# Kernel tuning notes

Measured on AMD Instinct MI355X. Metric: run time of the kernel, lower is better.

## Reference

```python
import jax, jax.numpy as jnp
import numpy as np

B, CIN, COUT, N = 8, 64, 64, 4096
MODES, L, M = 64, 100, 20


def _cc_nodes_weights(m):
    # Clenshaw-Curtis nodes cos(k*pi/n) and weights on [-1, 1]
    n = m - 1
    k = np.arange(m)
    nodes = np.cos(np.pi * k / n)
    v = np.ones(m)
    for j in range(1, n // 2 + 1):
        b = 1.0 if 2 * j == n else 2.0
        v -= b / (4.0 * j * j - 1.0) * np.cos(2.0 * j * k * np.pi / n)
    w = 2.0 * v / n
    w[0] *= 0.5
    w[-1] *= 0.5
    return nodes, w


def setup_inputs() -> dict:
    key = jax.random.key(0)
    k1, k2, k3 = jax.random.split(key, 3)
    scale = 1.0 / (CIN * COUT)
    x = jax.random.normal(k1, (B, CIN, N), dtype=jnp.float32)
    w_real = scale * jax.random.uniform(k2, (CIN, COUT, MODES), dtype=jnp.float32)
    w_imag = scale * jax.random.uniform(k3, (CIN, COUT, MODES), dtype=jnp.float32)
    return {"x": x, "w_real": w_real, "w_imag": w_imag}


def _forward(x, w_real, w_imag):
    b, c, n = x.shape
    t = jnp.linspace(0.0, 1.0, n)
    f = np.fft.fftfreq(n, d=1.0 / n).astype(np.float32)  # integer freqs, fft order
    nodes, cw = _cc_nodes_weights(M)

    # ---- CFT: X(f) = sum_{segments l, cheb nodes k} w_lk * x(t_lk) * exp(-2i*pi*f*t_lk)
    h = 0.5 / L                               # segment half-width on [0,1]
    cents = (np.arange(L) + 0.5) / L
    t_nodes = (cents[:, None] + h * nodes[None, :]).ravel().astype(np.float32)  # (L*M,)
    wts = np.broadcast_to(h * cw, (L, M)).ravel().astype(np.float32)            # (L*M,)
    tq = jnp.asarray(t_nodes)
    # interpolate each (b, c) signal onto the Chebyshev quadrature nodes
    xs = jax.vmap(lambda s: jnp.interp(tq, t, s))(x.reshape(b * c, n))  # (BC, LM)
    phase = -2.0 * jnp.pi * jnp.asarray(f)[:, None] * tq[None, :]       # (N, LM)
    E = jnp.exp(1j * phase).astype(jnp.complex64) * jnp.asarray(wts)[None, :]
    x_cft = (xs.astype(jnp.complex64) @ E.T).reshape(b, c, n)           # (B, Cin, N)

    # ---- spectral channel mixing on lowest MODES fft-order frequencies
    w = (w_real + 1j * w_imag).astype(jnp.complex64)
    out_low = jnp.einsum('bix,iox->box', x_cft[:, :, :MODES], w)
    out_ft = jnp.concatenate(
        [out_low, jnp.zeros((b, COUT, n - MODES), dtype=jnp.complex64)], axis=-1)

    # ---- ICFT: x(t) = int X(f) exp(+2i*pi*f*t) df via the same segment quadrature
    order = np.argsort(f)
    f_sorted = f[order]
    cs = out_ft[:, :, jnp.asarray(order)].reshape(b * COUT, n)
    fa, fb = float(f_sorted[0]), float(f_sorted[-1])
    hf = (fb - fa) / (2.0 * L)
    fc = fa + (np.arange(L) + 0.5) * (fb - fa) / L
    f_nodes = (fc[:, None] + hf * nodes[None, :]).ravel().astype(np.float32)
    wfs = np.broadcast_to(hf * cw, (L, M)).ravel().astype(np.float32)
    fq = jnp.asarray(f_nodes)
    fs = jnp.asarray(f_sorted)
    ci = jax.vmap(lambda cv: jnp.interp(fq, fs, cv.real)
                  + 1j * jnp.interp(fq, fs, cv.imag))(cs)               # (BC, LM)
    phase2 = 2.0 * jnp.pi * fq[:, None] * t[None, :]                     # (LM, N)
    E2 = jnp.exp(1j * phase2).astype(jnp.complex64) * jnp.asarray(wfs)[:, None]
    return (ci.astype(jnp.complex64) @ E2).real.reshape(b, COUT, n)


def reference(x, w_real, w_imag):
    return _forward(x, w_real, w_imag)
```

## Files before the change

### kernel.cpp

```cpp
#include <hip/hip_runtime.h>


#define NN 4096
#define C1_19 0.9863613034027223
#define NS3 33
#define NSP 40

#define OFF_XRE 0
#define OFF_XIM 32768
#define OFF_Z   65536

__device__ __forceinline__ float sin_rev(float r) { return __builtin_amdgcn_sinf(r); }
__device__ __forceinline__ float cos_rev(float r) { return __builtin_amdgcn_cosf(r); }

__device__ __forceinline__ void build_tables(double* nd, double* cwd, int t) {
    if (t == 0) {
        nd[0] = 1.0; nd[1] = C1_19;
        for (int k = 2; k < 20; ++k) nd[k] = 2.0 * C1_19 * nd[k - 1] - nd[k - 2];
    }
    __syncthreads();
    if (t < 20) {
        double v = 1.0;
        for (int j = 1; j <= 9; ++j) {
            int q = (2 * j * t) % 38; if (q > 19) q = 38 - q;
            v -= 2.0 / (4.0 * j * j - 1.0) * nd[q];
        }
        double w = 2.0 * v / 19.0;
        if (t == 0 || t == 19) w *= 0.5;
        cwd[t] = w;
    }
}

__global__ __launch_bounds__(256) void k_cft(const float* __restrict__ x,
                                             float* __restrict__ ws) {
    __shared__ double nd[20], cwd[20];
    __shared__ __align__(16) float xs[NN];
    __shared__ __align__(16) float xq[2000];
    __shared__ __align__(16) float Fri[20][64][2];
    __shared__ float red[4][64][2];
    const int t = threadIdx.x;
    const int bc = blockIdx.x;
    build_tables(nd, cwd, t);
#pragma unroll
    for (int it = 0; it < 4; ++it) {
        int c4 = it * 256 + t;
        *(float4*)&xs[c4 * 4] = *(const float4*)&x[(size_t)bc * NN + c4 * 4];
    }
    __syncthreads();
    for (int idx = t; idx < 1280; idx += 256) {
        int k = idx >> 6, m = idx & 63;
        double r = -0.005 * nd[k] * (double)m;
        r -= floor(r);
        float fr = (float)r;
        float w = (float)(0.005 * cwd[k]);
        Fri[k][m][0] = w * cos_rev(fr);
        Fri[k][m][1] = w * sin_rev(fr);
    }
#pragma unroll
    for (int it = 0; it < 8; ++it) {
        int node = it * 256 + t;
        if (node < 2000) {
            int l = node / 20, k = node - l * 20;
            double tq = 0.005 * ((double)(2 * l + 1) + nd[k]);
            double sf = tq * 4095.0;
            int i = (int)sf; if (i > 4094) i = 4094;
            double a = sf - (double)i;
            if (a < 0.0) a = 0.0; if (a > 1.0) a = 1.0;
            float af = (float)a;
            xq[node] = (1.f - af) * xs[i] + af * xs[i + 1];
        }
    }
    __syncthreads();
    const int m = t & 63, grp = t >> 6;
    float Fre[20], Fim[20];
#pragma unroll
    for (int k = 0; k < 20; ++k) {
        Fre[k] = Fri[k][m][0];
        Fim[k] = Fri[k][m][1];
    }
    float ar = 0.f, ai = 0.f;
    for (int l = grp * 25; l < grp * 25 + 25; ++l) {
        const float4* q4 = (const float4*)&xq[l * 20];
        float ur = 0.f, ui = 0.f;
#pragma unroll
        for (int c = 0; c < 5; ++c) {
            float4 q = q4[c];
            ur += q.x * Fre[c * 4]     + q.y * Fre[c * 4 + 1]
                + q.z * Fre[c * 4 + 2] + q.w * Fre[c * 4 + 3];
            ui += q.x * Fim[c * 4]     + q.y * Fim[c * 4 + 1]
                + q.z * Fim[c * 4 + 2] + q.w * Fim[c * 4 + 3];
        }
        double r = -(double)(m * (2 * l + 1)) / 200.0;
        r -= floor(r);
        float fr = (float)r;
        float tr = cos_rev(fr), ti = sin_rev(fr);
        ar += tr * ur - ti * ui;
        ai += tr * ui + ti * ur;
    }
    red[grp][m][0] = ar;
    red[grp][m][1] = ai;
    __syncthreads();
    if (t < 64) {
        float sr = (red[0][t][0] + red[1][t][0]) + (red[2][t][0] + red[3][t][0]);
        float si = (red[0][t][1] + red[1][t][1]) + (red[2][t][1] + red[3][t][1]);
        ws[OFF_XRE + (size_t)bc * 64 + t] = sr;
        ws[OFF_XIM + (size_t)bc * 64 + t] = si;
    }
}

__global__ __launch_bounds__(256) void k_mixZ(const float* __restrict__ wr,
                                              const float* __restrict__ wi,
                                              float* __restrict__ ws) {
    __shared__ double nd[20], cwd[20];
    __shared__ float part[4][2][64];
    __shared__ float yt[2][64];
    __shared__ float sw0[NS3], sw1[NS3];
    __shared__ int   si0[NS3], si1[NS3];
    const int t = threadIdx.x;
    const int b = blockIdx.x >> 6, o = blockIdx.x & 63;
    build_tables(nd, cwd, t);
    __syncthreads();
    if (t < NS3) {
        int l = (t < 2) ? 49 : (t < 22 ? 50 : 51);
        int k = (t < 2) ? t : (t < 22 ? t - 2 : t - 13);
        double fq = -2048.0 + ((double)l + 0.5) * 40.95 + 20.475 * nd[k];
        int m0 = (int)floor(fq);
        float fr = (float)(fq - (double)m0);
        sw0[t] = (m0 >= 0 && m0 <= 63) ? (1.f - fr) : 0.f;
        sw1[t] = (m0 + 1 >= 0 && m0 + 1 <= 63) ? fr : 0.f;
        si0[t] = min(max(m0, 0), 63);
        si1[t] = min(max(m0 + 1, 0), 63);
    }
    const int m = t & 63, grp = t >> 6;
    float yr = 0.f, yi = 0.f;
#pragma unroll 4
    for (int i = grp * 16; i < grp * 16 + 16; ++i) {
        float xr = ws[OFF_XRE + (size_t)(b * 64 + i) * 64 + m];
        float xi = ws[OFF_XIM + (size_t)(b * 64 + i) * 64 + m];
        float a = wr[((size_t)i * 64 + o) * 64 + m];
        float c = wi[((size_t)i * 64 + o) * 64 + m];
        yr += xr * a - xi * c;
        yi += xr * c + xi * a;
    }
    part[grp][0][m] = yr;
    part[grp][1][m] = yi;
    __syncthreads();
    if (t < 128) {
        int pr = t >> 6, mm = t & 63;
        yt[pr][mm] = ((part[0][pr][mm] + part[1][pr][mm]) +
                      (part[2][pr][mm] + part[3][pr][mm]));
    }
    __syncthreads();
    if (t < 2 * NS3) {
        int p = t >= NS3, s = t - p * NS3;
        float z = sw0[s] * yt[p][si0[s]] + sw1[s] * yt[p][si1[s]];
        ws[OFF_Z + (size_t)p * 512 * NSP + ((size_t)b * 64 + o) * NSP + s] = z;
    } else if (t < 2 * NS3 + 14) {
        int u = t - 2 * NS3;
        int p = u / 7, s = NS3 + u % 7;
        ws[OFF_Z + (size_t)p * 512 * NSP + ((size_t)b * 64 + o) * NSP + s] = 0.f;
    }
}

__global__ __launch_bounds__(256) void k_stage3(const float* __restrict__ ws,
                                                float* __restrict__ out) {
    __shared__ double nd[20], cwd[20];
    __shared__ double sfq[NS3];
    __shared__ float  swf[NS3];
    __shared__ __align__(16) float zt[2][64][41];
    __shared__ __align__(16) float e2[2][NSP][64];
    const int t = threadIdx.x;
    const int jt = blockIdx.x, pc = blockIdx.y;
    build_tables(nd, cwd, t);
    __syncthreads();
    if (t < NS3) {
        int l = (t < 2) ? 49 : (t < 22 ? 50 : 51);
        int k = (t < 2) ? t : (t < 22 ? t - 2 : t - 13);
        sfq[t] = -2048.0 + ((double)l + 0.5) * 40.95 + 20.475 * nd[k];
        swf[t] = (float)(20.475 * cwd[k]);
    }
    for (int idx = t; idx < 2 * 64 * NSP; idx += 256) {
        int part = idx / (64 * NSP), rem = idx % (64 * NSP);
        int row = rem / NSP, s = rem % NSP;
        zt[part][row][s] =
            ws[OFF_Z + (size_t)part * 512 * NSP + ((size_t)pc * 64 + row) * NSP + s];
    }
    __syncthreads();
    const double inv4095 = 1.0 / 4095.0;
    for (int idx = t; idx < NSP * 64; idx += 256) {
        int s = idx >> 6, jl = idx & 63;
        float cr = 0.f, ci = 0.f;
        if (s < NS3) {
            double ph = sfq[s] * ((double)(jt * 64 + jl) * inv4095);
            ph -= floor(ph);
            float fr = (float)ph;
            cr = swf[s] * cos_rev(fr);
            ci = swf[s] * sin_rev(fr);
        }
        e2[0][s][jl] = cr;
        e2[1][s][jl] = ci;
    }
    __syncthreads();
    const int jg = t & 15, pg = t >> 4;
    float acc[4][4] = {{0.f}};
    for (int s0 = 0; s0 < NSP; s0 += 8) {
        float zr[4][8], zi[4][8];
#pragma unroll
        for (int p = 0; p < 4; ++p)
#pragma unroll
            for (int u = 0; u < 8; ++u) {
                zr[p][u] = zt[0][pg * 4 + p][s0 + u];
                zi[p][u] = zt[1][pg * 4 + p][s0 + u];
            }
#pragma unroll
        for (int u = 0; u < 8; ++u) {
            const float4 er = *(const float4*)&e2[0][s0 + u][jg * 4];
            const float4 ei = *(const float4*)&e2[1][s0 + u][jg * 4];
#pragma unroll
            for (int p = 0; p < 4; ++p) {
                acc[p][0] += zr[p][u] * er.x - zi[p][u] * ei.x;
                acc[p][1] += zr[p][u] * er.y - zi[p][u] * ei.y;
                acc[p][2] += zr[p][u] * er.z - zi[p][u] * ei.z;
                acc[p][3] += zr[p][u] * er.w - zi[p][u] * ei.w;
            }
        }
    }
#pragma unroll
    for (int p = 0; p < 4; ++p) {
        float4 r;
        r.x = acc[p][0]; r.y = acc[p][1]; r.z = acc[p][2]; r.w = acc[p][3];
        *(float4*)&out[(size_t)(pc * 64 + pg * 4 + p) * NN + jt * 64 + jg * 4] = r;
    }
}

extern "C" void kernel_launch(void* const* d_in, const int* in_sizes, int n_in,
                              void* d_out, int out_size, void* d_ws, size_t ws_size,
                              hipStream_t stream) {
    const float* x  = (const float*)d_in[0];
    const float* wr = (const float*)d_in[1];
    const float* wi = (const float*)d_in[2];
    float* out = (float*)d_out;
    float* ws  = (float*)d_ws;
    (void)in_sizes; (void)n_in; (void)out_size; (void)ws_size;

    k_cft<<<512, 256, 0, stream>>>(x, ws);
    k_mixZ<<<512, 256, 0, stream>>>(wr, wi, ws);
    k_stage3<<<dim3(64, 8), 256, 0, stream>>>(ws, out);
}
```

Measured before the change: 31.10 us.

## Fuse channel-mixing and inverse-transform kernels with per-batch atomic counter barrier

Merges the mixing kernel and the inverse transform kernel into a single launch. Each block first computes its Z slice, then increments a per-batch counter and spins until all 64 blocks of that batch have arrived before running the inverse transform. This removes one kernel launch and its inter-kernel gap. Shared memory for the two phases is overlaid with a union. The counters are reset from the first kernel. Separately, the CFT twiddle phase now uses an integer modulo instead of double-precision floor. The spin barrier depends on all 512 blocks being co-resident and on correct memory visibility, since the stores and loads use only relaxed ordering.

```diff
diff --git a/kernel.cpp b/kernel.cpp
--- a/kernel.cpp
+++ b/kernel.cpp
@@ -9,6 +9,7 @@
 #define OFF_XRE 0
 #define OFF_XIM 32768
 #define OFF_Z   65536
+#define OFF_CNT 106496
 
 __device__ __forceinline__ float sin_rev(float r) { return __builtin_amdgcn_sinf(r); }
 __device__ __forceinline__ float cos_rev(float r) { return __builtin_amdgcn_cosf(r); }
@@ -40,6 +41,9 @@
     __shared__ float red[4][64][2];
     const int t = threadIdx.x;
     const int bc = blockIdx.x;
+    if (bc == 0 && t < 8)
+        __hip_atomic_store((unsigned*)ws + OFF_CNT + t * 16, 0u,
+                           __ATOMIC_RELAXED, __HIP_MEMORY_SCOPE_SYSTEM);
     build_tables(nd, cwd, t);
 #pragma unroll
     for (int it = 0; it < 4; ++it) {
@@ -90,10 +94,9 @@
             ui += q.x * Fim[c * 4]     + q.y * Fim[c * 4 + 1]
                 + q.z * Fim[c * 4 + 2] + q.w * Fim[c * 4 + 3];
         }
-        double r = -(double)(m * (2 * l + 1)) / 200.0;
-        r -= floor(r);
-        float fr = (float)r;
-        float tr = cos_rev(fr), ti = sin_rev(fr);
+        int u = (m * (2 * l + 1)) % 200;
+        float fr = (float)u * 0.005f;
+        float tr = cos_rev(fr), ti = -sin_rev(fr);
         ar += tr * ur - ti * ui;
         ai += tr * ui + ti * ur;
     }
@@ -108,22 +111,30 @@
     }
 }
 
-__global__ __launch_bounds__(256) void k_mixZ(const float* __restrict__ wr,
-                                              const float* __restrict__ wi,
-                                              float* __restrict__ ws) {
+struct PhC { float part[4][2][64]; float yt[2][64]; };
+struct PhD { float zt[2][64][41]; float e2[2][NSP][64]; };
+union SU2 { PhC c; PhD d; };
+
+__global__ __launch_bounds__(256) void k_mixicft(const float* __restrict__ wr,
+                                                 const float* __restrict__ wi,
+                                                 float* __restrict__ ws,
+                                                 float* __restrict__ out) {
+    __shared__ SU2 su;
     __shared__ double nd[20], cwd[20];
-    __shared__ float part[4][2][64];
-    __shared__ float yt[2][64];
     __shared__ float sw0[NS3], sw1[NS3];
     __shared__ int   si0[NS3], si1[NS3];
+    __shared__ double sfq[NS3];
+    __shared__ float  swf[NS3];
     const int t = threadIdx.x;
-    const int b = blockIdx.x >> 6, o = blockIdx.x & 63;
+    const int b = blockIdx.x >> 6, u = blockIdx.x & 63;
     build_tables(nd, cwd, t);
     __syncthreads();
     if (t < NS3) {
         int l = (t < 2) ? 49 : (t < 22 ? 50 : 51);
         int k = (t < 2) ? t : (t < 22 ? t - 2 : t - 13);
         double fq = -2048.0 + ((double)l + 0.5) * 40.95 + 20.475 * nd[k];
+        sfq[t] = fq;
+        swf[t] = (float)(20.475 * cwd[k]);
         int m0 = (int)floor(fq);
         float fr = (float)(fq - (double)m0);
         sw0[t] = (m0 >= 0 && m0 <= 63) ? (1.f - fr) : 0.f;
@@ -131,105 +142,104 @@
         si0[t] = min(max(m0, 0), 63);
         si1[t] = min(max(m0 + 1, 0), 63);
     }
-    const int m = t & 63, grp = t >> 6;
-    float yr = 0.f, yi = 0.f;
+    {
+        const int o = u;
+        const int m = t & 63, grp = t >> 6;
+        float yr = 0.f, yi = 0.f;
 #pragma unroll 4
-    for (int i = grp * 16; i < grp * 16 + 16; ++i) {
-        float xr = ws[OFF_XRE + (size_t)(b * 64 + i) * 64 + m];
-        float xi = ws[OFF_XIM + (size_t)(b * 64 + i) * 64 + m];
-        float a = wr[((size_t)i * 64 + o) * 64 + m];
-        float c = wi[((size_t)i * 64 + o) * 64 + m];
-        yr += xr * a - xi * c;
-        yi += xr * c + xi * a;
-    }
-    part[grp][0][m] = yr;
-    part[grp][1][m] = yi;
-    __syncthreads();
-    if (t < 128) {
-        int pr = t >> 6, mm = t & 63;
-        yt[pr][mm] = ((part[0][pr][mm] + part[1][pr][mm]) +
-                      (part[2][pr][mm] + part[3][pr][mm]));
-    }
-    __syncthreads();
-    if (t < 2 * NS3) {
-        int p = t >= NS3, s = t - p * NS3;
-        float z = sw0[s] * yt[p][si0[s]] + sw1[s] * yt[p][si1[s]];
-        ws[OFF_Z + (size_t)p * 512 * NSP + ((size_t)b * 64 + o) * NSP + s] = z;
-    } else if (t < 2 * NS3 + 14) {
-        int u = t - 2 * NS3;
-        int p = u / 7, s = NS3 + u % 7;
-        ws[OFF_Z + (size_t)p * 512 * NSP + ((size_t)b * 64 + o) * NSP + s] = 0.f;
-    }
-}
-
-__global__ __launch_bounds__(256) void k_stage3(const float* __restrict__ ws,
-                                                float* __restrict__ out) {
-    __shared__ double nd[20], cwd[20];
-    __shared__ double sfq[NS3];
-    __shared__ float  swf[NS3];
-    __shared__ __align__(16) float zt[2][64][41];
-    __shared__ __align__(16) float e2[2][NSP][64];
-    const int t = threadIdx.x;
-    const int jt = blockIdx.x, pc = blockIdx.y;
-    build_tables(nd, cwd, t);
-    __syncthreads();
-    if (t < NS3) {
-        int l = (t < 2) ? 49 : (t < 22 ? 50 : 51);
-        int k = (t < 2) ? t : (t < 22 ? t - 2 : t - 13);
-        sfq[t] = -2048.0 + ((double)l + 0.5) * 40.95 + 20.475 * nd[k];
-        swf[t] = (float)(20.475 * cwd[k]);
-    }
-    for (int idx = t; idx < 2 * 64 * NSP; idx += 256) {
-        int part = idx / (64 * NSP), rem = idx % (64 * NSP);
-        int row = rem / NSP, s = rem % NSP;
-        zt[part][row][s] =
-            ws[OFF_Z + (size_t)part * 512 * NSP + ((size_t)pc * 64 + row) * NSP + s];
-    }
-    __syncthreads();
-    const double inv4095 = 1.0 / 4095.0;
-    for (int idx = t; idx < NSP * 64; idx += 256) {
-        int s = idx >> 6, jl = idx & 63;
-        float cr = 0.f, ci = 0.f;
-        if (s < NS3) {
-            double ph = sfq[s] * ((double)(jt * 64 + jl) * inv4095);
-            ph -= floor(ph);
-            float fr = (float)ph;
-            cr = swf[s] * cos_rev(fr);
-            ci = swf[s] * sin_rev(fr);
-        }
-        e2[0][s][jl] = cr;
-        e2[1][s][jl] = ci;
-    }
-    __syncthreads();
-    const int jg = t & 15, pg = t >> 4;
-    float acc[4][4] = {{0.f}};
-    for (int s0 = 0; s0 < NSP; s0 += 8) {
-        float zr[4][8], zi[4][8];
-#pragma unroll
-        for (int p = 0; p < 4; ++p)
-#pragma unroll
-            for (int u = 0; u < 8; ++u) {
-                zr[p][u] = zt[0][pg * 4 + p][s0 + u];
-                zi[p][u] = zt[1][pg * 4 + p][s0 + u];
+        for (int i = grp * 16; i < grp * 16 + 16; ++i) {
+            float xr = ws[OFF_XRE + (size_t)(b * 64 + i) * 64 + m];
+            float xi = ws[OFF_XIM + (size_t)(b * 64 + i) * 64 + m];
+            float a = wr[((size_t)i * 64 + o) * 64 + m];
+            float c = wi[((size_t)i * 64 + o) * 64 + m];
+            yr += xr * a - xi * c;
+            yi += xr * c + xi * a;
+        }
+        su.c.part[grp][0][m] = yr;
+        su.c.part[grp][1][m] = yi;
+        __syncthreads();
+        if (t < 128) {
+            int pr = t >> 6, mm = t & 63;
+            su.c.yt[pr][mm] = ((su.c.part[0][pr][mm] + su.c.part[1][pr][mm]) +
+                               (su.c.part[2][pr][mm] + su.c.part[3][pr][mm]));
+        }
+        __syncthreads();
+        if (t < 2 * NS3) {
+            int p = t >= NS3, s = t - p * NS3;
+            float z = sw0[s] * su.c.yt[p][si0[s]] + sw1[s] * su.c.yt[p][si1[s]];
+            __hip_atomic_store(&ws[OFF_Z + (size_t)p * 512 * NSP +
+                                   ((size_t)b * 64 + o) * NSP + s],
+                               z, __ATOMIC_RELAXED, __HIP_MEMORY_SCOPE_SYSTEM);
+        } else if (t < 2 * NS3 + 14) {
+            int q = t - 2 * NS3;
+            int p = q / 7, s = NS3 + q % 7;
+            __hip_atomic_store(&ws[OFF_Z + (size_t)p * 512 * NSP +
+                                   ((size_t)b * 64 + o) * NSP + s],
+                               0.f, __ATOMIC_RELAXED, __HIP_MEMORY_SCOPE_SYSTEM);
+        }
+    }
+    __syncthreads();
+    if (t == 0) {
+        unsigned* cnt = (unsigned*)ws + OFF_CNT + b * 16;
+        __hip_atomic_fetch_add(cnt, 1u, __ATOMIC_RELAXED, __HIP_MEMORY_SCOPE_AGENT);
+        while (__hip_atomic_load(cnt, __ATOMIC_RELAXED, __HIP_MEMORY_SCOPE_AGENT) < 64u)
+            __builtin_amdgcn_s_sleep(4);
+    }
+    __syncthreads();
+    {
+        const int jt = u, pc = b;
+        for (int idx = t; idx < 2 * 64 * NSP; idx += 256) {
+            int part = idx / (64 * NSP), rem = idx % (64 * NSP);
+            int row = rem / NSP, s = rem % NSP;
+            su.d.zt[part][row][s] =
+                ws[OFF_Z + (size_t)part * 512 * NSP + ((size_t)pc * 64 + row) * NSP + s];
+        }
+        __syncthreads();
+        const double inv4095 = 1.0 / 4095.0;
+        for (int idx = t; idx < NSP * 64; idx += 256) {
+            int s = idx >> 6, jl = idx & 63;
+            float cr = 0.f, ci = 0.f;
+            if (s < NS3) {
+                double ph = sfq[s] * ((double)(jt * 64 + jl) * inv4095);
+                ph -= floor(ph);
+                float fr = (float)ph;
+                cr = swf[s] * cos_rev(fr);
+                ci = swf[s] * sin_rev(fr);
             }
-#pragma unroll
-        for (int u = 0; u < 8; ++u) {
-            const float4 er = *(const float4*)&e2[0][s0 + u][jg * 4];
-            const float4 ei = *(const float4*)&e2[1][s0 + u][jg * 4];
-#pragma unroll
-            for (int p = 0; p < 4; ++p) {
-                acc[p][0] += zr[p][u] * er.x - zi[p][u] * ei.x;
-                acc[p][1] += zr[p][u] * er.y - zi[p][u] * ei.y;
-                acc[p][2] += zr[p][u] * er.z - zi[p][u] * ei.z;
-                acc[p][3] += zr[p][u] * er.w - zi[p][u] * ei.w;
+            su.d.e2[0][s][jl] = cr;
+            su.d.e2[1][s][jl] = ci;
+        }
+        __syncthreads();
+        const int jg = t & 15, pg = t >> 4;
+        float acc[4][4] = {{0.f}};
+        for (int s0 = 0; s0 < NSP; s0 += 8) {
+            float zr[4][8], zi[4][8];
+#pragma unroll
+            for (int p = 0; p < 4; ++p)
+#pragma unroll
+                for (int v = 0; v < 8; ++v) {
+                    zr[p][v] = su.d.zt[0][pg * 4 + p][s0 + v];
+                    zi[p][v] = su.d.zt[1][pg * 4 + p][s0 + v];
+                }
+#pragma unroll
+            for (int v = 0; v < 8; ++v) {
+                const float4 er = *(const float4*)&su.d.e2[0][s0 + v][jg * 4];
+                const float4 ei = *(const float4*)&su.d.e2[1][s0 + v][jg * 4];
+#pragma unroll
+                for (int p = 0; p < 4; ++p) {
+                    acc[p][0] += zr[p][v] * er.x - zi[p][v] * ei.x;
+                    acc[p][1] += zr[p][v] * er.y - zi[p][v] * ei.y;
+                    acc[p][2] += zr[p][v] * er.z - zi[p][v] * ei.z;
+                    acc[p][3] += zr[p][v] * er.w - zi[p][v] * ei.w;
+                }
             }
         }
-    }
-#pragma unroll
-    for (int p = 0; p < 4; ++p) {
-        float4 r;
-        r.x = acc[p][0]; r.y = acc[p][1]; r.z = acc[p][2]; r.w = acc[p][3];
-        *(float4*)&out[(size_t)(pc * 64 + pg * 4 + p) * NN + jt * 64 + jg * 4] = r;
+#pragma unroll
+        for (int p = 0; p < 4; ++p) {
+            float4 r;
+            r.x = acc[p][0]; r.y = acc[p][1]; r.z = acc[p][2]; r.w = acc[p][3];
+            *(float4*)&out[(size_t)(pc * 64 + pg * 4 + p) * NN + jt * 64 + jg * 4] = r;
+        }
     }
 }
 
@@ -244,6 +254,5 @@
     (void)in_sizes; (void)n_in; (void)out_size; (void)ws_size;
 
     k_cft<<<512, 256, 0, stream>>>(x, ws);
-    k_mixZ<<<512, 256, 0, stream>>>(wr, wi, ws);
-    k_stage3<<<dim3(64, 8), 256, 0, stream>>>(ws, out);
-}
+    k_mixicft<<<512, 256, 0, stream>>>(wr, wi, ws, out);
+}
```

New measurement: 35.34 us. 13.6% more time.

## Split CFT and ICFT work across more blocks to raise parallelism

Applied to the files above, without the earlier changes.

The CFT kernel is split into two half-signal blocks per (b,c) row. Each block loads half of the input and handles 50 segments, and the two partial spectra are written to separate workspace halves and summed in the mixing kernel. The ICFT kernel is retiled to 32-column output tiles with 2 rows per thread, doubling the grid to 1024 blocks. The segment phase now uses integer modular arithmetic in place of double-precision floor. This gives more blocks to fill the GPU, at the cost of extra workspace traffic, repeated table setup per block, and a smaller per-thread register tile.

```diff
diff --git a/kernel.cpp b/kernel.cpp
--- a/kernel.cpp
+++ b/kernel.cpp
@@ -8,7 +8,7 @@
 
 #define OFF_XRE 0
 #define OFF_XIM 32768
-#define OFF_Z   65536
+#define OFF_Z   131072
 
 __device__ __forceinline__ float sin_rev(float r) { return __builtin_amdgcn_sinf(r); }
 __device__ __forceinline__ float cos_rev(float r) { return __builtin_amdgcn_cosf(r); }
@@ -34,18 +34,16 @@
 __global__ __launch_bounds__(256) void k_cft(const float* __restrict__ x,
                                              float* __restrict__ ws) {
     __shared__ double nd[20], cwd[20];
-    __shared__ __align__(16) float xs[NN];
-    __shared__ __align__(16) float xq[2000];
+    __shared__ __align__(16) float xs[2052];
+    __shared__ __align__(16) float xq[1000];
     __shared__ __align__(16) float Fri[20][64][2];
     __shared__ float red[4][64][2];
     const int t = threadIdx.x;
-    const int bc = blockIdx.x;
+    const int bc = blockIdx.x, h = blockIdx.y;
+    const int i0 = h ? 2044 : 0;
     build_tables(nd, cwd, t);
-#pragma unroll
-    for (int it = 0; it < 4; ++it) {
-        int c4 = it * 256 + t;
-        *(float4*)&xs[c4 * 4] = *(const float4*)&x[(size_t)bc * NN + c4 * 4];
-    }
+    for (int idx = t; idx < 513; idx += 256)
+        *(float4*)&xs[idx * 4] = *(const float4*)&x[(size_t)bc * NN + i0 + idx * 4];
     __syncthreads();
     for (int idx = t; idx < 1280; idx += 256) {
         int k = idx >> 6, m = idx & 63;
@@ -56,19 +54,16 @@
         Fri[k][m][0] = w * cos_rev(fr);
         Fri[k][m][1] = w * sin_rev(fr);
     }
-#pragma unroll
-    for (int it = 0; it < 8; ++it) {
-        int node = it * 256 + t;
-        if (node < 2000) {
-            int l = node / 20, k = node - l * 20;
-            double tq = 0.005 * ((double)(2 * l + 1) + nd[k]);
-            double sf = tq * 4095.0;
-            int i = (int)sf; if (i > 4094) i = 4094;
-            double a = sf - (double)i;
-            if (a < 0.0) a = 0.0; if (a > 1.0) a = 1.0;
-            float af = (float)a;
-            xq[node] = (1.f - af) * xs[i] + af * xs[i + 1];
-        }
+    for (int idx = t; idx < 1000; idx += 256) {
+        int l_loc = idx / 20, k = idx - l_loc * 20;
+        int l = h * 50 + l_loc;
+        double tq = 0.005 * ((double)(2 * l + 1) + nd[k]);
+        double sf = tq * 4095.0;
+        int i = (int)sf; if (i > 4094) i = 4094;
+        double a = sf - (double)i;
+        if (a < 0.0) a = 0.0; if (a > 1.0) a = 1.0;
+        float af = (float)a;
+        xq[idx] = (1.f - af) * xs[i - i0] + af * xs[i - i0 + 1];
     }
     __syncthreads();
     const int m = t & 63, grp = t >> 6;
@@ -79,8 +74,8 @@
         Fim[k] = Fri[k][m][1];
     }
     float ar = 0.f, ai = 0.f;
-    for (int l = grp * 25; l < grp * 25 + 25; ++l) {
-        const float4* q4 = (const float4*)&xq[l * 20];
+    for (int l_loc = grp; l_loc < 50; l_loc += 4) {
+        const float4* q4 = (const float4*)&xq[l_loc * 20];
         float ur = 0.f, ui = 0.f;
 #pragma unroll
         for (int c = 0; c < 5; ++c) {
@@ -90,10 +85,10 @@
             ui += q.x * Fim[c * 4]     + q.y * Fim[c * 4 + 1]
                 + q.z * Fim[c * 4 + 2] + q.w * Fim[c * 4 + 3];
         }
-        double r = -(double)(m * (2 * l + 1)) / 200.0;
-        r -= floor(r);
-        float fr = (float)r;
-        float tr = cos_rev(fr), ti = sin_rev(fr);
+        int l = h * 50 + l_loc;
+        int u = (m * (2 * l + 1)) % 200;
+        float fr = (float)u * 0.005f;
+        float tr = cos_rev(fr), ti = -sin_rev(fr);
         ar += tr * ur - ti * ui;
         ai += tr * ui + ti * ur;
     }
@@ -103,14 +98,15 @@
     if (t < 64) {
         float sr = (red[0][t][0] + red[1][t][0]) + (red[2][t][0] + red[3][t][0]);
         float si = (red[0][t][1] + red[1][t][1]) + (red[2][t][1] + red[3][t][1]);
-        ws[OFF_XRE + (size_t)bc * 64 + t] = sr;
-        ws[OFF_XIM + (size_t)bc * 64 + t] = si;
-    }
-}
-
-__global__ __launch_bounds__(256) void k_mixZ(const float* __restrict__ wr,
-                                              const float* __restrict__ wi,
-                                              float* __restrict__ ws) {
+        const int base = h * 65536;
+        ws[base + OFF_XRE + (size_t)bc * 64 + t] = sr;
+        ws[base + OFF_XIM + (size_t)bc * 64 + t] = si;
+    }
+}
+
+__global__ __launch_bounds__(256) void k_mix(const float* __restrict__ wr,
+                                             const float* __restrict__ wi,
+                                             float* __restrict__ ws) {
     __shared__ double nd[20], cwd[20];
     __shared__ float part[4][2][64];
     __shared__ float yt[2][64];
@@ -135,8 +131,9 @@
     float yr = 0.f, yi = 0.f;
 #pragma unroll 4
     for (int i = grp * 16; i < grp * 16 + 16; ++i) {
-        float xr = ws[OFF_XRE + (size_t)(b * 64 + i) * 64 + m];
-        float xi = ws[OFF_XIM + (size_t)(b * 64 + i) * 64 + m];
+        const size_t off = (size_t)(b * 64 + i) * 64 + m;
+        float xr = ws[OFF_XRE + off] + ws[65536 + OFF_XRE + off];
+        float xi = ws[OFF_XIM + off] + ws[65536 + OFF_XIM + off];
         float a = wr[((size_t)i * 64 + o) * 64 + m];
         float c = wi[((size_t)i * 64 + o) * 64 + m];
         yr += xr * a - xi * c;
@@ -156,21 +153,21 @@
         float z = sw0[s] * yt[p][si0[s]] + sw1[s] * yt[p][si1[s]];
         ws[OFF_Z + (size_t)p * 512 * NSP + ((size_t)b * 64 + o) * NSP + s] = z;
     } else if (t < 2 * NS3 + 14) {
-        int u = t - 2 * NS3;
-        int p = u / 7, s = NS3 + u % 7;
+        int q = t - 2 * NS3;
+        int p = q / 7, s = NS3 + q % 7;
         ws[OFF_Z + (size_t)p * 512 * NSP + ((size_t)b * 64 + o) * NSP + s] = 0.f;
     }
 }
 
-__global__ __launch_bounds__(256) void k_stage3(const float* __restrict__ ws,
-                                                float* __restrict__ out) {
+__global__ __launch_bounds__(256) void k_icft(const float* __restrict__ ws,
+                                              float* __restrict__ out) {
     __shared__ double nd[20], cwd[20];
     __shared__ double sfq[NS3];
     __shared__ float  swf[NS3];
     __shared__ __align__(16) float zt[2][64][41];
-    __shared__ __align__(16) float e2[2][NSP][64];
+    __shared__ __align__(16) float e2[2][NSP][36];
     const int t = threadIdx.x;
-    const int jt = blockIdx.x, pc = blockIdx.y;
+    const int jt2 = blockIdx.x, pc = blockIdx.y;
     build_tables(nd, cwd, t);
     __syncthreads();
     if (t < NS3) {
@@ -187,49 +184,50 @@
     }
     __syncthreads();
     const double inv4095 = 1.0 / 4095.0;
-    for (int idx = t; idx < NSP * 64; idx += 256) {
-        int s = idx >> 6, jl = idx & 63;
+    for (int idx = t; idx < NSP * 32; idx += 256) {
+        int s = idx >> 5, jl = idx & 31;
         float cr = 0.f, ci = 0.f;
         if (s < NS3) {
-            double ph = sfq[s] * ((double)(jt * 64 + jl) * inv4095);
+            double ph = sfq[s] * ((double)(jt2 * 32 + jl) * inv4095);
             ph -= floor(ph);
             float fr = (float)ph;
             cr = swf[s] * cos_rev(fr);
             ci = swf[s] * sin_rev(fr);
         }
+        e2[0][s][jl + (jl >> 3) * 0] = cr;
+        e2[1][s][jl] = ci;
         e2[0][s][jl] = cr;
-        e2[1][s][jl] = ci;
-    }
-    __syncthreads();
-    const int jg = t & 15, pg = t >> 4;
-    float acc[4][4] = {{0.f}};
+    }
+    __syncthreads();
+    const int jg = t & 7, pg = t >> 3;
+    float acc[2][4] = {{0.f}};
     for (int s0 = 0; s0 < NSP; s0 += 8) {
-        float zr[4][8], zi[4][8];
-#pragma unroll
-        for (int p = 0; p < 4; ++p)
-#pragma unroll
-            for (int u = 0; u < 8; ++u) {
-                zr[p][u] = zt[0][pg * 4 + p][s0 + u];
-                zi[p][u] = zt[1][pg * 4 + p][s0 + u];
+        float zr[2][8], zi[2][8];
+#pragma unroll
+        for (int p = 0; p < 2; ++p)
+#pragma unroll
+            for (int v = 0; v < 8; ++v) {
+                zr[p][v] = zt[0][pg * 2 + p][s0 + v];
+                zi[p][v] = zt[1][pg * 2 + p][s0 + v];
             }
 #pragma unroll
-        for (int u = 0; u < 8; ++u) {
-            const float4 er = *(const float4*)&e2[0][s0 + u][jg * 4];
-            const float4 ei = *(const float4*)&e2[1][s0 + u][jg * 4];
-#pragma unroll
-            for (int p = 0; p < 4; ++p) {
-                acc[p][0] += zr[p][u] * er.x - zi[p][u] * ei.x;
-                acc[p][1] += zr[p][u] * er.y - zi[p][u] * ei.y;
-                acc[p][2] += zr[p][u] * er.z - zi[p][u] * ei.z;
-                acc[p][3] += zr[p][u] * er.w - zi[p][u] * ei.w;
+        for (int v = 0; v < 8; ++v) {
+            const float4 er = *(const float4*)&e2[0][s0 + v][jg * 4];
+            const float4 ei = *(const float4*)&e2[1][s0 + v][jg * 4];
+#pragma unroll
+            for (int p = 0; p < 2; ++p) {
+                acc[p][0] += zr[p][v] * er.x - zi[p][v] * ei.x;
+                acc[p][1] += zr[p][v] * er.y - zi[p][v] * ei.y;
+                acc[p][2] += zr[p][v] * er.z - zi[p][v] * ei.z;
+                acc[p][3] += zr[p][v] * er.w - zi[p][v] * ei.w;
             }
         }
     }
 #pragma unroll
-    for (int p = 0; p < 4; ++p) {
+    for (int p = 0; p < 2; ++p) {
         float4 r;
         r.x = acc[p][0]; r.y = acc[p][1]; r.z = acc[p][2]; r.w = acc[p][3];
-        *(float4*)&out[(size_t)(pc * 64 + pg * 4 + p) * NN + jt * 64 + jg * 4] = r;
+        *(float4*)&out[(size_t)(pc * 64 + pg * 2 + p) * NN + jt2 * 32 + jg * 4] = r;
     }
 }
 
@@ -243,7 +241,7 @@
     float* ws  = (float*)d_ws;
     (void)in_sizes; (void)n_in; (void)out_size; (void)ws_size;
 
-    k_cft<<<512, 256, 0, stream>>>(x, ws);
-    k_mixZ<<<512, 256, 0, stream>>>(wr, wi, ws);
-    k_stage3<<<dim3(64, 8), 256, 0, stream>>>(ws, out);
-}
+    k_cft<<<dim3(512, 2), 256, 0, stream>>>(x, ws);
+    k_mix<<<512, 256, 0, stream>>>(wr, wi, ws);
+    k_icft<<<dim3(128, 8), 256, 0, stream>>>(ws, out);
+}
```

Result: no change. 31.17 us (+0.3%).
